# Kernel optimization log

Measured on AMD Instinct MI355X. Metric: run time of the kernel, lower is better.

## Reference

```python
import jax, jax.numpy as jnp
import numpy as np

N = 100000      # nodes
K = 16          # fixed degree (num_ngbrs)
E = N * K       # edges
NFEAT = 128
NHID = 64
OPFEAT = 64


def setup_inputs() -> dict:
    key = jax.random.key(0)
    ks = jax.random.split(key, 8)
    x = jax.random.normal(ks[0], (N, NFEAT), dtype=jnp.float32)
    # edges sorted by destination node, exactly K per node (required by the
    # original e.view(-1, num_ngbrs) softmax reshape)
    edge_row = jnp.repeat(jnp.arange(N, dtype=jnp.int32), K)
    edge_col = jax.random.randint(ks[1], (E,), 0, N, dtype=jnp.int32)
    stdv1 = 1.0 / np.sqrt(NHID)
    stdv2 = 1.0 / np.sqrt(OPFEAT)
    W1 = jax.random.uniform(ks[2], (NFEAT, NHID), jnp.float32, -stdv1, stdv1)
    b1 = jax.random.uniform(ks[3], (NHID,), jnp.float32, -stdv1, stdv1)
    a1 = jax.random.normal(ks[4], (2 * NHID,), jnp.float32) * 0.1
    W2 = jax.random.uniform(ks[5], (NHID, OPFEAT), jnp.float32, -stdv2, stdv2)
    b2 = jax.random.uniform(ks[6], (OPFEAT,), jnp.float32, -stdv2, stdv2)
    a2 = jax.random.normal(ks[7], (2 * OPFEAT,), jnp.float32) * 0.1
    return {"x": x, "edge_row": edge_row, "edge_col": edge_col,
            "W1": W1, "a1": a1, "b1": b1, "W2": W2, "a2": a2, "b2": b2,
            "k": K}


def _gat_layer(x, W, a, b, edge_row, edge_col, k):
    n = x.shape[0]
    h = x @ W                                        # [N, F_out]
    # edge score: concat(h[dst], h[src]) . a  -> leaky_relu
    h_edge = jnp.concatenate([h[edge_row], h[edge_col]], axis=1)  # [E, 2F]
    e = jax.nn.leaky_relu(h_edge @ a, negative_slope=0.2)         # [E]
    # per-destination softmax over the fixed K neighbors (edges row-sorted)
    att = jax.nn.softmax(e.reshape(-1, k), axis=1).reshape(-1)    # [E]
    att = jax.lax.stop_gradient(att)  # original detaches attention
    # sparse (adj * attention) @ h  ==  segment-sum of att_e * h[src_e]
    out = jax.ops.segment_sum(att[:, None] * h[edge_col], edge_row,
                              num_segments=n)
    return out + b


def reference(x, edge_row, edge_col, W1, a1, b1, W2, a2, b2, k):
    x1 = jax.nn.relu(_gat_layer(x, W1, a1, b1, edge_row, edge_col, k))
    x2 = jax.nn.relu(_gat_layer(x1, W2, a2, b2, edge_row, edge_col, k))
    return x2
```

## Files before the change

kernel.cpp:

```cpp
#include <hip/hip_runtime.h>


typedef __attribute__((ext_vector_type(8))) _Float16 f16x8;
typedef __attribute__((ext_vector_type(4))) _Float16 f16x4;
typedef __attribute__((ext_vector_type(4))) float floatx4;

static __device__ inline float ubitf(unsigned u) { union { unsigned u; float f; } v; v.u = u; return v.f; }
static __device__ inline unsigned fbitu(float f) { union { float f; unsigned u; } v; v.f = f; return v.u; }

template<int KD>
__global__ __launch_bounds__(256, 2) void gemm_score_f16(
    const float* __restrict__ X, const float* __restrict__ W,
    const float* __restrict__ av, _Float16* __restrict__ H,
    float* __restrict__ s1, float* __restrict__ s2, int n)
{
    constexpr int NKT = KD / 32;
    constexpr int NF = NKT * 4 * 64;
    __shared__ f16x8 Bs[NF];
    const int tid = threadIdx.x;

    for (int f = tid; f < NF; f += 256) {
        const int ln = f & 63, ntk = f >> 6;
        const int kt = ntk >> 2, nt = ntk & 3;
        const int kbase = kt * 32 + (ln >> 4) * 8;
        const int ccol = nt * 16 + (ln & 15);
        f16x8 hh;
#pragma unroll
        for (int j = 0; j < 8; j++)
            hh[j] = (_Float16)W[(kbase + j) * 64 + ccol];
        Bs[f] = hh;
    }
    __syncthreads();

    const int wave = tid >> 6, lane = tid & 63;
    const int quad = lane >> 4, l15 = lane & 15;
    const int r0 = blockIdx.x * 192 + wave * 48;

    float a1c[4], a2c[4];
#pragma unroll
    for (int nt = 0; nt < 4; nt++) {
        a1c[nt] = av[nt * 16 + l15];
        a2c[nt] = av[64 + nt * 16 + l15];
    }

    float4 raw[NKT][3][2];
#pragma unroll
    for (int rb = 0; rb < 3; rb++) {
        int ra = r0 + rb * 16 + l15; if (ra > n - 1) ra = n - 1;
        const float* xp = &X[(size_t)ra * KD + quad * 8];
#pragma unroll
        for (int kt = 0; kt < NKT; kt++) {
            raw[kt][rb][0] = *(const float4*)(xp + kt * 32);
            raw[kt][rb][1] = *(const float4*)(xp + kt * 32 + 4);
        }
    }
    f16x8 A[NKT][3];
#pragma unroll
    for (int kt = 0; kt < NKT; kt++)
#pragma unroll
        for (int rb = 0; rb < 3; rb++) {
            f16x8 a;
            a[0] = (_Float16)raw[kt][rb][0].x; a[1] = (_Float16)raw[kt][rb][0].y;
            a[2] = (_Float16)raw[kt][rb][0].z; a[3] = (_Float16)raw[kt][rb][0].w;
            a[4] = (_Float16)raw[kt][rb][1].x; a[5] = (_Float16)raw[kt][rb][1].y;
            a[6] = (_Float16)raw[kt][rb][1].z; a[7] = (_Float16)raw[kt][rb][1].w;
            A[kt][rb] = a;
        }

    floatx4 acc[4][3];
#pragma unroll
    for (int nt = 0; nt < 4; nt++)
#pragma unroll
        for (int rb = 0; rb < 3; rb++) acc[nt][rb] = (floatx4){0, 0, 0, 0};

#pragma unroll
    for (int kt = 0; kt < NKT; kt++)
#pragma unroll
        for (int nt = 0; nt < 4; nt++) {
            const f16x8 b = Bs[(kt * 4 + nt) * 64 + lane];
#pragma unroll
            for (int rb = 0; rb < 3; rb++)
                acc[nt][rb] = __builtin_amdgcn_mfma_f32_16x16x32_f16(A[kt][rb], b, acc[nt][rb], 0, 0, 0);
        }

#pragma unroll
    for (int rb = 0; rb < 3; rb++) {
        float p1[4] = {0, 0, 0, 0}, p2[4] = {0, 0, 0, 0};
#pragma unroll
        for (int nt = 0; nt < 4; nt++)
#pragma unroll
            for (int reg = 0; reg < 4; reg++) {
                const int r = r0 + rb * 16 + quad * 4 + reg;
                if (r < n) H[(size_t)r * 64 + nt * 16 + l15] = (_Float16)acc[nt][rb][reg];
                p1[reg] = fmaf(acc[nt][rb][reg], a1c[nt], p1[reg]);
                p2[reg] = fmaf(acc[nt][rb][reg], a2c[nt], p2[reg]);
            }
#pragma unroll
        for (int m = 1; m < 16; m <<= 1)
#pragma unroll
            for (int reg = 0; reg < 4; reg++) {
                p1[reg] += __shfl_xor(p1[reg], m, 64);
                p2[reg] += __shfl_xor(p2[reg], m, 64);
            }
        if (l15 == 0)
#pragma unroll
            for (int reg = 0; reg < 4; reg++) {
                const int r = r0 + rb * 16 + quad * 4 + reg;
                if (r < n) { s1[r] = p1[reg]; s2[r] = p2[reg]; }
            }
    }
}

__global__ __launch_bounds__(256, 2) void gemm2_score(
    const _Float16* __restrict__ Xm, const float* __restrict__ W,
    const float* __restrict__ av, _Float16* __restrict__ H,
    float* __restrict__ s1, float* __restrict__ s2, int n)
{
    constexpr int NKT = 2;
    constexpr int NF = NKT * 4 * 64;
    __shared__ f16x8 Bs[NF];
    const int tid = threadIdx.x;

    for (int f = tid; f < NF; f += 256) {
        const int ln = f & 63, ntk = f >> 6;
        const int kt = ntk >> 2, nt = ntk & 3;
        const int kbase = kt * 32 + (ln >> 4) * 8;
        const int ccol = nt * 16 + (ln & 15);
        f16x8 hh;
#pragma unroll
        for (int j = 0; j < 8; j++)
            hh[j] = (_Float16)W[(kbase + j) * 64 + ccol];
        Bs[f] = hh;
    }
    __syncthreads();

    const int wave = tid >> 6, lane = tid & 63;
    const int quad = lane >> 4, l15 = lane & 15;
    const int r0 = blockIdx.x * 192 + wave * 48;

    f16x8 br[NKT][4];
#pragma unroll
    for (int kt = 0; kt < NKT; kt++)
#pragma unroll
        for (int nt = 0; nt < 4; nt++)
            br[kt][nt] = Bs[(kt * 4 + nt) * 64 + lane];

    float a1c[4], a2c[4];
#pragma unroll
    for (int nt = 0; nt < 4; nt++) {
        a1c[nt] = av[nt * 16 + l15];
        a2c[nt] = av[64 + nt * 16 + l15];
    }

    f16x8 A[NKT][3];
#pragma unroll
    for (int rb = 0; rb < 3; rb++) {
        int ra = r0 + rb * 16 + l15; if (ra > n - 1) ra = n - 1;
        const _Float16* xp = &Xm[(size_t)ra * 64 + quad * 8];
#pragma unroll
        for (int kt = 0; kt < NKT; kt++)
            A[kt][rb] = *(const f16x8*)(xp + kt * 32);
    }

    floatx4 acc[4][3];
#pragma unroll
    for (int nt = 0; nt < 4; nt++)
#pragma unroll
        for (int rb = 0; rb < 3; rb++) acc[nt][rb] = (floatx4){0, 0, 0, 0};

#pragma unroll
    for (int kt = 0; kt < NKT; kt++)
#pragma unroll
        for (int nt = 0; nt < 4; nt++)
#pragma unroll
            for (int rb = 0; rb < 3; rb++)
                acc[nt][rb] = __builtin_amdgcn_mfma_f32_16x16x32_f16(A[kt][rb], br[kt][nt], acc[nt][rb], 0, 0, 0);

#pragma unroll
    for (int rb = 0; rb < 3; rb++) {
        float p1[4] = {0, 0, 0, 0}, p2[4] = {0, 0, 0, 0};
#pragma unroll
        for (int nt = 0; nt < 4; nt++)
#pragma unroll
            for (int reg = 0; reg < 4; reg++) {
                const int r = r0 + rb * 16 + quad * 4 + reg;
                if (r < n) H[(size_t)r * 64 + nt * 16 + l15] = (_Float16)acc[nt][rb][reg];
                p1[reg] = fmaf(acc[nt][rb][reg], a1c[nt], p1[reg]);
                p2[reg] = fmaf(acc[nt][rb][reg], a2c[nt], p2[reg]);
            }
#pragma unroll
        for (int m = 1; m < 16; m <<= 1)
#pragma unroll
            for (int reg = 0; reg < 4; reg++) {
                p1[reg] += __shfl_xor(p1[reg], m, 64);
                p2[reg] += __shfl_xor(p2[reg], m, 64);
            }
        if (l15 == 0)
#pragma unroll
            for (int reg = 0; reg < 4; reg++) {
                const int r = r0 + rb * 16 + quad * 4 + reg;
                if (r < n) { s1[r] = p1[reg]; s2[r] = p2[reg]; }
            }
    }
}

template<typename OT>
__global__ __launch_bounds__(512) void attn(
    const _Float16* __restrict__ H, const float* __restrict__ s1,
    const float* __restrict__ s2, const int* __restrict__ col,
    const float* __restrict__ bias, OT* __restrict__ out, int n)
{
    const int lane = threadIdx.x & 63;
    const int wv = threadIdx.x >> 6;
    const int j = lane & 15;
    const int dst = blockIdx.x * 32 + wv * 4 + (lane >> 4);
    if (dst >= n) return;

    const int c = col[dst * 16 + j];
    float e = s1[dst] + s2[c];
    e = (e > 0.0f) ? e : 0.2f * e;
    float m = e;
#pragma unroll
    for (int mk = 1; mk < 16; mk <<= 1) m = fmaxf(m, __shfl_xor(m, mk, 64));
    float p = __expf(e - m);
    float s = p;
#pragma unroll
    for (int mk = 1; mk < 16; mk <<= 1) s += __shfl_xor(s, mk, 64);
    const float att = p / s;

    const int bbase = (lane & 48) << 2;
    int srck[16]; float attk[16];
#pragma unroll
    for (int k = 0; k < 16; k++) {
        const int bidx = bbase + (k << 2);
        srck[k] = __builtin_amdgcn_ds_bpermute(bidx, c);
        attk[k] = ubitf((unsigned)__builtin_amdgcn_ds_bpermute(bidx, (int)fbitu(att)));
    }
    f16x4 hv[16];
#pragma unroll
    for (int k = 0; k < 16; k++)
        hv[k] = *(const f16x4*)&H[(size_t)srck[k] * 64 + j * 4];

    float a0 = 0, a1 = 0, a2 = 0, a3 = 0;
#pragma unroll
    for (int k = 0; k < 16; k++) {
        a0 = fmaf(attk[k], (float)hv[k][0], a0);
        a1 = fmaf(attk[k], (float)hv[k][1], a1);
        a2 = fmaf(attk[k], (float)hv[k][2], a2);
        a3 = fmaf(attk[k], (float)hv[k][3], a3);
    }
    const float4 bv = *(const float4*)&bias[j * 4];
    const float o0 = fmaxf(a0 + bv.x, 0.0f);
    const float o1 = fmaxf(a1 + bv.y, 0.0f);
    const float o2 = fmaxf(a2 + bv.z, 0.0f);
    const float o3 = fmaxf(a3 + bv.w, 0.0f);
    if constexpr (sizeof(OT) == 2) {
        f16x4 o; o[0] = (_Float16)o0; o[1] = (_Float16)o1;
                 o[2] = (_Float16)o2; o[3] = (_Float16)o3;
        *(f16x4*)&out[(size_t)dst * 64 + j * 4] = o;
    } else {
        float4 o; o.x = o0; o.y = o1; o.z = o2; o.w = o3;
        *(float4*)&out[(size_t)dst * 64 + j * 4] = o;
    }
}

extern "C" void kernel_launch(void* const* d_in, const int* in_sizes, int n_in,
                              void* d_out, int out_size, void* d_ws, size_t ws_size,
                              hipStream_t stream)
{
    const float* x        = (const float*)d_in[0];
    const int*   edge_col = (const int*)  d_in[2];
    const float* W1       = (const float*)d_in[3];
    const float* a1       = (const float*)d_in[4];
    const float* b1       = (const float*)d_in[5];
    const float* W2       = (const float*)d_in[6];
    const float* a2       = (const float*)d_in[7];
    const float* b2       = (const float*)d_in[8];
    const int n = in_sizes[0] / 128;

    _Float16* h1 = (_Float16*)d_ws;
    _Float16* xm = h1 + (size_t)n * 64;
    _Float16* h2 = xm + (size_t)n * 64;
    float* s1a = (float*)(h2 + (size_t)n * 64);
    float* s2a = s1a + n;
    float* s1b = s2a + n;
    float* s2b = s1b + n;

    const int gemm_blocks = (n + 191) / 192;
    const int agg_blocks  = (n + 31) / 32;

    gemm_score_f16<128><<<gemm_blocks, 256, 0, stream>>>(x, W1, a1, h1, s1a, s2a, n);
    attn<_Float16><<<agg_blocks, 512, 0, stream>>>(h1, s1a, s2a, edge_col, b1, xm, n);
    gemm2_score<<<gemm_blocks, 256, 0, stream>>>(xm, W2, a2, h2, s1b, s2b, n);
    attn<float><<<agg_blocks, 512, 0, stream>>>(h2, s1b, s2b, edge_col, b2, (float*)d_out, n);
}
```

Before: 184.0 us.

## Remap attention aggregation to 8 lanes per node with 16-byte gathers

The attention/aggregation kernel now assigns 8 lanes per destination node instead of 16, so each lane gathers 8 half-precision features (16-byte loads) per neighbor and handles two edges for the softmax. The H gathers are issued before the score/softmax computation so the load latency can overlap with the exp/shuffle work. Out-of-range nodes are clamped instead of returning early, and blocks now cover 64 nodes each. The wider per-lane accumulators raise register use, which may reduce occupancy.

```diff
diff --git a/kernel.cpp b/kernel.cpp
--- a/kernel.cpp
+++ b/kernel.cpp
@@ -2,7 +2,6 @@
 
 
 typedef __attribute__((ext_vector_type(8))) _Float16 f16x8;
-typedef __attribute__((ext_vector_type(4))) _Float16 f16x4;
 typedef __attribute__((ext_vector_type(4))) float floatx4;
 
 static __device__ inline float ubitf(unsigned u) { union { unsigned u; float f; } v; v.u = u; return v.f; }
@@ -212,55 +211,77 @@
 {
     const int lane = threadIdx.x & 63;
     const int wv = threadIdx.x >> 6;
-    const int j = lane & 15;
-    const int dst = blockIdx.x * 32 + wv * 4 + (lane >> 4);
-    if (dst >= n) return;
-
-    const int c = col[dst * 16 + j];
-    float e = s1[dst] + s2[c];
-    e = (e > 0.0f) ? e : 0.2f * e;
-    float m = e;
-#pragma unroll
-    for (int mk = 1; mk < 16; mk <<= 1) m = fmaxf(m, __shfl_xor(m, mk, 64));
-    float p = __expf(e - m);
-    float s = p;
-#pragma unroll
-    for (int mk = 1; mk < 16; mk <<= 1) s += __shfl_xor(s, mk, 64);
-    const float att = p / s;
-
-    const int bbase = (lane & 48) << 2;
-    int srck[16]; float attk[16];
-#pragma unroll
-    for (int k = 0; k < 16; k++) {
-        const int bidx = bbase + (k << 2);
-        srck[k] = __builtin_amdgcn_ds_bpermute(bidx, c);
-        attk[k] = ubitf((unsigned)__builtin_amdgcn_ds_bpermute(bidx, (int)fbitu(att)));
-    }
-    f16x4 hv[16];
+    const int g = lane >> 3, j = lane & 7;
+    const int dst = blockIdx.x * 64 + wv * 8 + g;
+    const int dc = (dst > n - 1) ? (n - 1) : dst;
+
+    const int c0 = col[dc * 16 + j];
+    const int c1 = col[dc * 16 + 8 + j];
+
+    const int bb4 = (lane & 56) << 2;
+    int srck[16];
+#pragma unroll
+    for (int k = 0; k < 8; k++) {
+        srck[k]     = __builtin_amdgcn_ds_bpermute(bb4 + 4 * k, c0);
+        srck[k + 8] = __builtin_amdgcn_ds_bpermute(bb4 + 4 * k, c1);
+    }
+    f16x8 hv[16];
 #pragma unroll
     for (int k = 0; k < 16; k++)
-        hv[k] = *(const f16x4*)&H[(size_t)srck[k] * 64 + j * 4];
-
-    float a0 = 0, a1 = 0, a2 = 0, a3 = 0;
-#pragma unroll
-    for (int k = 0; k < 16; k++) {
-        a0 = fmaf(attk[k], (float)hv[k][0], a0);
-        a1 = fmaf(attk[k], (float)hv[k][1], a1);
-        a2 = fmaf(attk[k], (float)hv[k][2], a2);
-        a3 = fmaf(attk[k], (float)hv[k][3], a3);
-    }
-    const float4 bv = *(const float4*)&bias[j * 4];
-    const float o0 = fmaxf(a0 + bv.x, 0.0f);
-    const float o1 = fmaxf(a1 + bv.y, 0.0f);
-    const float o2 = fmaxf(a2 + bv.z, 0.0f);
-    const float o3 = fmaxf(a3 + bv.w, 0.0f);
-    if constexpr (sizeof(OT) == 2) {
-        f16x4 o; o[0] = (_Float16)o0; o[1] = (_Float16)o1;
-                 o[2] = (_Float16)o2; o[3] = (_Float16)o3;
-        *(f16x4*)&out[(size_t)dst * 64 + j * 4] = o;
-    } else {
-        float4 o; o.x = o0; o.y = o1; o.z = o2; o.w = o3;
-        *(float4*)&out[(size_t)dst * 64 + j * 4] = o;
+        hv[k] = *(const f16x8*)&H[(size_t)srck[k] * 64 + j * 8];
+
+    const float s1d = s1[dc];
+    float e0 = s1d + s2[c0];
+    float e1 = s1d + s2[c1];
+    e0 = (e0 > 0.0f) ? e0 : 0.2f * e0;
+    e1 = (e1 > 0.0f) ? e1 : 0.2f * e1;
+    float m = fmaxf(e0, e1);
+    m = fmaxf(m, __shfl_xor(m, 1, 64));
+    m = fmaxf(m, __shfl_xor(m, 2, 64));
+    m = fmaxf(m, __shfl_xor(m, 4, 64));
+    const float p0 = __expf(e0 - m), p1 = __expf(e1 - m);
+    float s = p0 + p1;
+    s += __shfl_xor(s, 1, 64); s += __shfl_xor(s, 2, 64); s += __shfl_xor(s, 4, 64);
+    const float inv = 1.0f / s;
+    const float att0 = p0 * inv, att1 = p1 * inv;
+
+    float attk[16];
+#pragma unroll
+    for (int k = 0; k < 8; k++) {
+        attk[k]     = ubitf((unsigned)__builtin_amdgcn_ds_bpermute(bb4 + 4 * k, (int)fbitu(att0)));
+        attk[k + 8] = ubitf((unsigned)__builtin_amdgcn_ds_bpermute(bb4 + 4 * k, (int)fbitu(att1)));
+    }
+
+    float acc[8] = {0, 0, 0, 0, 0, 0, 0, 0};
+#pragma unroll
+    for (int k = 0; k < 16; k++)
+#pragma unroll
+        for (int q = 0; q < 8; q++)
+            acc[q] = fmaf(attk[k], (float)hv[k][q], acc[q]);
+
+    if (dst < n) {
+        float4 b0 = *(const float4*)&bias[j * 8];
+        float4 b1 = *(const float4*)&bias[j * 8 + 4];
+        const float o0 = fmaxf(acc[0] + b0.x, 0.0f);
+        const float o1 = fmaxf(acc[1] + b0.y, 0.0f);
+        const float o2 = fmaxf(acc[2] + b0.z, 0.0f);
+        const float o3 = fmaxf(acc[3] + b0.w, 0.0f);
+        const float o4 = fmaxf(acc[4] + b1.x, 0.0f);
+        const float o5 = fmaxf(acc[5] + b1.y, 0.0f);
+        const float o6 = fmaxf(acc[6] + b1.z, 0.0f);
+        const float o7 = fmaxf(acc[7] + b1.w, 0.0f);
+        if constexpr (sizeof(OT) == 2) {
+            f16x8 o;
+            o[0] = (_Float16)o0; o[1] = (_Float16)o1; o[2] = (_Float16)o2; o[3] = (_Float16)o3;
+            o[4] = (_Float16)o4; o[5] = (_Float16)o5; o[6] = (_Float16)o6; o[7] = (_Float16)o7;
+            *(f16x8*)&out[(size_t)dst * 64 + j * 8] = o;
+        } else {
+            float4 w0, w1;
+            w0.x = o0; w0.y = o1; w0.z = o2; w0.w = o3;
+            w1.x = o4; w1.y = o5; w1.z = o6; w1.w = o7;
+            *(float4*)&out[(size_t)dst * 64 + j * 8] = w0;
+            *(float4*)&out[(size_t)dst * 64 + j * 8 + 4] = w1;
+        }
     }
 }
 
@@ -287,7 +308,7 @@
     float* s2b = s1b + n;
 
     const int gemm_blocks = (n + 191) / 192;
-    const int agg_blocks  = (n + 31) / 32;
+    const int agg_blocks  = (n + 63) / 64;
 
     gemm_score_f16<128><<<gemm_blocks, 256, 0, stream>>>(x, W1, a1, h1, s1a, s2a, n);
     attn<_Float16><<<agg_blocks, 512, 0, stream>>>(h1, s1a, s2a, edge_col, b1, xm, n);
```

Measured after the change: 190.6 us. 3.6% more time.
